# Kernel optimization log

Measured on AMD Instinct MI355X. Metric: run time of the kernel, lower is better.

The kernel has to match this reference:

```python
import jax, jax.numpy as jnp
import numpy as np

SEQ, BATCH, D_MODEL = 128, 64, 2048
D_STATE, D_CONV, CHUNK = 16, 4, 32
D_INNER = int(1.2 * D_MODEL)      # 2457
GROUPS = 7                        # largest g<=8 dividing 2457
DT_RANK = max(4, D_MODEL // 64)   # 32
WIN = 8
NEG = -1e30


def setup_inputs() -> dict:
    key = jax.random.key(0)
    ks = jax.random.split(key, 8)
    w = lambda k, shape, s: (jax.random.normal(k, shape) * s).astype(jnp.float32)
    return {
        "x": jax.random.normal(ks[0], (SEQ, BATCH, D_MODEL), dtype=jnp.float32),
        "W_in": w(ks[1], (D_INNER, D_MODEL), 0.02),
        "b_in": jnp.zeros((D_INNER,), jnp.float32),
        "W_gate": w(ks[2], (D_INNER, D_MODEL), 0.02),
        "b_gate": jnp.zeros((D_INNER,), jnp.float32),
        "W_conv": w(ks[3], (D_INNER, D_INNER // GROUPS, D_CONV), 0.05),
        "b_conv": jnp.zeros((D_INNER,), jnp.float32),
        "W_xproj": w(ks[4], (DT_RANK + D_STATE, D_INNER), 0.02),
        "b_xproj": jnp.zeros((DT_RANK + D_STATE,), jnp.float32),
        "W_dt": w(ks[5], (D_INNER, DT_RANK), 0.1),
        "Dparam": jnp.full((D_INNER,), 0.1, jnp.float32),
        "W_out": w(ks[6], (D_MODEL, D_INNER), 0.02),
        "b_out": jnp.zeros((D_MODEL,), jnp.float32),
        "ln_w": jnp.ones((D_MODEL,), jnp.float32),
        "ln_b": jnp.zeros((D_MODEL,), jnp.float32),
    }


def reference(x, W_in, b_in, W_gate, b_gate, W_conv, b_conv,
              W_xproj, b_xproj, W_dt, Dparam, W_out, b_out, ln_w, ln_b):
    def process_chunk(xc_in):                      # [L, B, d_model]
        L = xc_in.shape[0]
        xi = xc_in @ W_in.T + b_in                 # [L, B, d_inner]
        z = xc_in @ W_gate.T + b_gate              # gate
        # causal grouped conv1d: torch pads both sides by d_conv-1 then
        # truncates [:L]  ==  left-pad (d_conv-1), VALID conv
        c = jnp.transpose(xi, (1, 2, 0))           # [B, d_inner, L]
        c = jnp.pad(c, ((0, 0), (0, 0), (D_CONV - 1, 0)))
        c = jax.lax.conv_general_dilated(
            c, W_conv, window_strides=(1,), padding='VALID',
            dimension_numbers=('NCH', 'OIH', 'NCH'),
            feature_group_count=GROUPS) + b_conv[None, :, None]
        xc = jax.nn.silu(jnp.transpose(c, (2, 0, 1)))   # [L, B, d_inner]
        # dt_t = softplus(dt_proj(x_proj(x_t)[:dt_rank])) + 1e-4
        xp = xc @ W_xproj.T + b_xproj
        dt = jax.nn.softplus(xp[..., :DT_RANK] @ W_dt.T) + 1e-4  # [L,B,d_inner]
        xpad = jnp.pad(xc, ((WIN - 1, 0), (0, 0), (0, 0)))
        windows = jnp.stack([xpad[k:k + L] for k in range(WIN)], axis=1)
        t = jnp.arange(L)
        kk = jnp.arange(WIN)
        offset = jnp.maximum(0, WIN - 1 - t)       # shift so arange starts at 0
        ar = kk[None, :] - offset[:, None]
        valid = ar >= 0
        logits = dt[:, None] * ar[:, :, None, None].astype(dt.dtype)
        logits = jnp.where(valid[:, :, None, None], logits, NEG)
        wgt = jax.nn.softmax(logits, axis=1)       # softmax over window
        local = jnp.sum(wgt * windows, axis=1)     # [L, B, d_inner]
        return (local + Dparam * xc) * jax.nn.sigmoid(z)

    # chunks are processed independently (window + conv restart per chunk)
    xr = x.reshape(SEQ // CHUNK, CHUNK, BATCH, D_MODEL)
    ys = jax.vmap(process_chunk)(xr).reshape(SEQ, BATCH, D_INNER)
    compressed = ys[-WIN:].mean(axis=0)            # mean of last 8 steps
    out = compressed @ W_out.T + b_out             # [B, d_model]
    mu = out.mean(-1, keepdims=True)
    var = ((out - mu) ** 2).mean(-1, keepdims=True)
    return ((out - mu) / jnp.sqrt(var + 1e-5)) * ln_w + ln_b
```

## Files before the change

kernel.cpp:

```cpp
#include <hip/hip_runtime.h>
#include <math.h>
#include <stdint.h>

#define DMODEL 2048
#define DINNER 2457
#define NI     2464
#define GROUPS 7
#define GCH    351
#define GP     352
#define GNP    384
#define NROW_XI 1152
#define NROW_Z  512
#define NCAT   5120
#define GATE0  2560
#define OUT_SPLITS 16
#define CONV_PLANE (GROUPS * GNP * GP)

typedef __attribute__((ext_vector_type(8))) __bf16 bf16x8;
typedef __attribute__((ext_vector_type(4))) float f32x4;
typedef __attribute__((ext_vector_type(8))) unsigned short ushort8;

__device__ inline unsigned short f2bf(float f) {
    union { float f; unsigned int u; } v; v.f = f;
    unsigned int u = v.u;
    return (unsigned short)((u + 0x7FFFu + ((u >> 16) & 1u)) >> 16);
}

__device__ inline int lds_addr(int row, int slot) {
    return row * 32 + ((slot ^ ((row >> 1) & 3)) << 3);
}

__device__ __forceinline__ void gload16(const unsigned short* g, unsigned short* l) {
    __builtin_amdgcn_global_load_lds(
        (const __attribute__((address_space(1))) unsigned int*)g,
        (__attribute__((address_space(3))) unsigned int*)l, 16, 0, 0);
}

#define CAST_B0 1152
#define CAST_B1 6066
#define CAST_B2 9435
__global__ __launch_bounds__(256)
void cast_all(const float* __restrict__ x110,
              const float* __restrict__ Win, const float* __restrict__ Wg,
              const float* __restrict__ Wc,
              unsigned short* __restrict__ A_x,
              unsigned short* __restrict__ B_cat,
              unsigned short* __restrict__ B_cv)
{
    int bx = blockIdx.x;
    if (bx < CAST_B0) {
        size_t t = (size_t)bx * 256 + threadIdx.x;
        const float4* s = (const float4*)x110 + t * 2;
        float4 a = s[0], b = s[1];
        ushort8 o;
        o[0]=f2bf(a.x); o[1]=f2bf(a.y); o[2]=f2bf(a.z); o[3]=f2bf(a.w);
        o[4]=f2bf(b.x); o[5]=f2bf(b.y); o[6]=f2bf(b.z); o[7]=f2bf(b.w);
        *(ushort8*)(A_x + t * 8) = o;
    } else if (bx < CAST_B1) {
        int idx = bx - CAST_B0;
        int half = idx >= DINNER;
        int cb = half ? idx - DINNER : idx;
        const float* src = half ? Wg : Win;
        size_t t = (size_t)cb * 256 + threadIdx.x;
        size_t elem = t * 8;
        size_t doff = elem + (half ? (size_t)GATE0 * DMODEL : 0);
        const float4* s = (const float4*)(src + elem);
        float4 a = s[0], b = s[1];
        ushort8 o;
        o[0]=f2bf(a.x); o[1]=f2bf(a.y); o[2]=f2bf(a.z); o[3]=f2bf(a.w);
        o[4]=f2bf(b.x); o[5]=f2bf(b.y); o[6]=f2bf(b.z); o[7]=f2bf(b.w);
        *(ushort8*)(B_cat + doff) = o;
    } else {
        int t = (bx - CAST_B1) * 256 + threadIdx.x;
        if (t >= DINNER * GCH) return;
        int oc = t / GCH, i = t - oc * GCH;
        float4 w = *(const float4*)(Wc + (size_t)t * 4);
        int g = oc / GCH, ol = oc - g * GCH;
        size_t base = (size_t)(g * GNP + ol) * GP + i;
        B_cv[0 * (size_t)CONV_PLANE + base] = f2bf(w.x);
        B_cv[1 * (size_t)CONV_PLANE + base] = f2bf(w.y);
        B_cv[2 * (size_t)CONV_PLANE + base] = f2bf(w.z);
        B_cv[3 * (size_t)CONV_PLANE + base] = f2bf(w.w);
        if (i == GCH - 1) {
            B_cv[0 * (size_t)CONV_PLANE + base + 1] = 0;
            B_cv[1 * (size_t)CONV_PLANE + base + 1] = 0;
            B_cv[2 * (size_t)CONV_PLANE + base + 1] = 0;
            B_cv[3 * (size_t)CONV_PLANE + base + 1] = 0;
        }
    }
}

#define NKF 64
__global__ __launch_bounds__(256)
void gemm_mfma_fused(const unsigned short* __restrict__ A,
                     const unsigned short* __restrict__ B,
                     const float* __restrict__ b_in,
                     const float* __restrict__ b_gate,
                     unsigned short* __restrict__ xi,
                     float* __restrict__ zb)
{
    __shared__ unsigned short sm[5 * 256 * 32];
    const int tid = threadIdx.x;
    const int w = tid >> 6, l = tid & 63;
    const int l15 = l & 15, l4 = l >> 4;
    const int wm = w >> 1, wn = w & 1;

    const int orig = blockIdx.x;
    const int xcd = orig & 7, lo = orig >> 3;
    const int logical = (xcd < 4 ? xcd * 33 : 132 + (xcd - 4) * 32) + lo;
    int mt, nt, is_gate;
    if (logical < 180) { nt = logical / 9; mt = logical % 9; is_gate = 0; }
    else { int b2 = logical - 180; nt = 20 + b2 / 4; mt = 5 + b2 % 4; is_gate = 1; }
    const int m0 = mt * 128, n0 = nt * 128;

    const int lr = l >> 2, slot = l & 3;
    const int r0 = w * 16 + lr, r1 = r0 + 64;
    const int xo0 = (slot ^ ((r0 >> 1) & 3)) << 3;
    const int xo1 = (slot ^ ((r1 >> 1) & 3)) << 3;
    const unsigned short* gA0 = A + (size_t)(m0 + r0) * DMODEL + xo0;
    const unsigned short* gA1 = A + (size_t)(m0 + r1) * DMODEL + xo1;
    const unsigned short* gB0 = B + (size_t)(n0 + r0) * DMODEL + xo0;
    const unsigned short* gB1 = B + (size_t)(n0 + r1) * DMODEL + xo1;
    unsigned short* dA0 = sm + w * 512;
    unsigned short* dA1 = sm + (w + 4) * 512;
    unsigned short* dB0 = sm + 4096 + w * 512;
    unsigned short* dB1 = sm + 4096 + (w + 4) * 512;

#define STAGE_G(buf, ks) do { int _o = (ks) * 32, _b = (buf) * 8192; \
    gload16(gA0 + _o, dA0 + _b); gload16(gA1 + _o, dA1 + _b); \
    gload16(gB0 + _o, dB0 + _b); gload16(gB1 + _o, dB1 + _b); } while (0)

    f32x4 acc[4][4] = {};
    auto compute = [&](const unsigned short* base) {
        bf16x8 af[4], bfr[4];
#pragma unroll
        for (int f = 0; f < 4; ++f)
            af[f] = *(const bf16x8*)(base + lds_addr(wm * 64 + f * 16 + l15, l4));
#pragma unroll
        for (int j = 0; j < 4; ++j)
            bfr[j] = *(const bf16x8*)(base + 4096 + lds_addr(wn * 64 + j * 16 + l15, l4));
        __builtin_amdgcn_s_setprio(1);
#pragma unroll
        for (int i = 0; i < 4; ++i)
#pragma unroll
            for (int j = 0; j < 4; ++j)
                acc[i][j] = __builtin_amdgcn_mfma_f32_16x16x32_bf16(af[i], bfr[j], acc[i][j], 0, 0, 0);
        __builtin_amdgcn_s_setprio(0);
    };

    STAGE_G(0, 0); STAGE_G(1, 1); STAGE_G(2, 2); STAGE_G(3, 3);
    int rbuf = 0, sbuf = 4;
    for (int ks = 0; ks < NKF - 4; ++ks) {
        asm volatile("s_waitcnt vmcnt(12)" ::: "memory");
        __builtin_amdgcn_s_barrier();
        STAGE_G(sbuf, ks + 4);
        compute(sm + rbuf * 8192);
        rbuf = rbuf == 4 ? 0 : rbuf + 1;
        sbuf = sbuf == 4 ? 0 : sbuf + 1;
    }
    asm volatile("s_waitcnt vmcnt(12)" ::: "memory");
    __builtin_amdgcn_s_barrier();
    compute(sm + rbuf * 8192); rbuf = rbuf == 4 ? 0 : rbuf + 1;
    asm volatile("s_waitcnt vmcnt(8)" ::: "memory");
    __builtin_amdgcn_s_barrier();
    compute(sm + rbuf * 8192); rbuf = rbuf == 4 ? 0 : rbuf + 1;
    asm volatile("s_waitcnt vmcnt(4)" ::: "memory");
    __builtin_amdgcn_s_barrier();
    compute(sm + rbuf * 8192); rbuf = rbuf == 4 ? 0 : rbuf + 1;
    asm volatile("s_waitcnt vmcnt(0)" ::: "memory");
    __builtin_amdgcn_s_barrier();
    compute(sm + rbuf * 8192);
#undef STAGE_G

    if (!is_gate) {
#pragma unroll
        for (int j = 0; j < 4; ++j) {
            int colg = n0 + wn * 64 + j * 16 + l15;
            if (colg < DINNER) {
                int g = colg / GCH, ci = colg - g * GCH;
                float bias = b_in[colg];
                size_t dco = (size_t)(g * GP + ci);
#pragma unroll
                for (int i = 0; i < 4; ++i)
#pragma unroll
                    for (int r = 0; r < 4; ++r) {
                        int row = m0 + wm * 64 + i * 16 + l4 * 4 + r;
                        xi[(size_t)row * NI + dco] = f2bf(acc[i][j][r] + bias);
                        if (ci == GCH - 1) xi[(size_t)row * NI + dco + 1] = 0;
                    }
            }
        }
    } else {
#pragma unroll
        for (int j = 0; j < 4; ++j) {
            int ng = n0 + wn * 64 + j * 16 + l15 - GATE0;
            if (ng < DINNER) {
                float bias = b_gate[ng];
#pragma unroll
                for (int i = 0; i < 4; ++i)
#pragma unroll
                    for (int r = 0; r < 4; ++r) {
                        int row = m0 + wm * 64 + i * 16 + l4 * 4 + r;
                        zb[(size_t)(row - 640) * NI + ng] = acc[i][j][r] + bias;
                    }
            }
        }
    }
}

#define NKC 44
__global__ __launch_bounds__(256)
void conv_mfma(const unsigned short* __restrict__ xi,
               const unsigned short* __restrict__ Bc,
               const float* __restrict__ bc,
               float* __restrict__ xcb)
{
    __shared__ unsigned short sm[5 * 192 * 32];
    const int tid = threadIdx.x;
    const int w = tid >> 6, l = tid & 63;
    const int l15 = l & 15, l4 = l >> 4;
    const int wm = w >> 1, wn = w & 1;

    const int orig = blockIdx.x;
    const int xcd = orig & 7, lo = orig >> 3;
    const int logical = (xcd < 3 ? xcd * 40 : 120 + (xcd - 3) * 39) + lo;
    const int gn = logical / 15, mt = logical % 15;
    const int g = gn / 3, nt = gn % 3;
    const int m0 = mt * 64;
    const int n0l = nt * 128;

    const int lr = l >> 2, slot = l & 3;
    const int rA = w * 16 + lr;
    const int rB1 = rA + 64;
    const int xoA  = (slot ^ ((rA  >> 1) & 3)) << 3;
    const int xoB1 = (slot ^ ((rB1 >> 1) & 3)) << 3;
    const unsigned short* gAb = xi + (size_t)(m0 + rA) * NI + g * GP + xoA;
    const unsigned short* gB0 = Bc + (size_t)(g * GNP + n0l + rA) * GP + xoA;
    const unsigned short* gB1 = Bc + (size_t)(g * GNP + n0l + rB1) * GP + xoB1;
    unsigned short* dA  = sm + w * 512;
    unsigned short* dB0 = sm + 2048 + w * 512;
    unsigned short* dB1 = sm + 2048 + (w + 4) * 512;

#define STAGE_C(buf, ks) do { \
    int _tap = (ks) / 11, _kc = (ks) - _tap * 11, _b = (buf) * 6144; \
    size_t _ao = (size_t)(64 * _tap) * NI + _kc * 32; \
    size_t _bo = (size_t)_tap * CONV_PLANE + _kc * 32; \
    gload16(gAb + _ao, dA  + _b); \
    gload16(gB0 + _bo, dB0 + _b); \
    gload16(gB1 + _bo, dB1 + _b); } while (0)

    f32x4 acc[2][4] = {};
    auto compute = [&](const unsigned short* base) {
        bf16x8 af[2], bfr[4];
#pragma unroll
        for (int f = 0; f < 2; ++f)
            af[f] = *(const bf16x8*)(base + lds_addr(wm * 32 + f * 16 + l15, l4));
#pragma unroll
        for (int j = 0; j < 4; ++j)
            bfr[j] = *(const bf16x8*)(base + 2048 + lds_addr(wn * 64 + j * 16 + l15, l4));
        __builtin_amdgcn_s_setprio(1);
#pragma unroll
        for (int i = 0; i < 2; ++i)
#pragma unroll
            for (int j = 0; j < 4; ++j)
                acc[i][j] = __builtin_amdgcn_mfma_f32_16x16x32_bf16(af[i], bfr[j], acc[i][j], 0, 0, 0);
        __builtin_amdgcn_s_setprio(0);
    };

    STAGE_C(0, 0); STAGE_C(1, 1); STAGE_C(2, 2); STAGE_C(3, 3);
    int rbuf = 0, sbuf = 4;
    for (int ks = 0; ks < NKC - 4; ++ks) {
        asm volatile("s_waitcnt vmcnt(9)" ::: "memory");
        __builtin_amdgcn_s_barrier();
        STAGE_C(sbuf, ks + 4);
        compute(sm + rbuf * 6144);
        rbuf = rbuf == 4 ? 0 : rbuf + 1;
        sbuf = sbuf == 4 ? 0 : sbuf + 1;
    }
    asm volatile("s_waitcnt vmcnt(9)" ::: "memory");
    __builtin_amdgcn_s_barrier();
    compute(sm + rbuf * 6144); rbuf = rbuf == 4 ? 0 : rbuf + 1;
    asm volatile("s_waitcnt vmcnt(6)" ::: "memory");
    __builtin_amdgcn_s_barrier();
    compute(sm + rbuf * 6144); rbuf = rbuf == 4 ? 0 : rbuf + 1;
    asm volatile("s_waitcnt vmcnt(3)" ::: "memory");
    __builtin_amdgcn_s_barrier();
    compute(sm + rbuf * 6144); rbuf = rbuf == 4 ? 0 : rbuf + 1;
    asm volatile("s_waitcnt vmcnt(0)" ::: "memory");
    __builtin_amdgcn_s_barrier();
    compute(sm + rbuf * 6144);
#undef STAGE_C

#pragma unroll
    for (int j = 0; j < 4; ++j) {
        int ocl = n0l + wn * 64 + j * 16 + l15;
        if (ocl < GCH) {
            int ch = g * GCH + ocl;
            float bias = bc[ch];
#pragma unroll
            for (int i = 0; i < 2; ++i)
#pragma unroll
                for (int r = 0; r < 4; ++r) {
                    int row = m0 + wm * 32 + i * 16 + l4 * 4 + r;
                    float v = acc[i][j][r] + bias;
                    xcb[(size_t)row * NI + ch] = v / (1.f + expf(-v));
                }
        }
    }
}

__global__ __launch_bounds__(256)
void xp_kernel(const float* __restrict__ xc,
               const float* __restrict__ Wxp,
               const float* __restrict__ bxp,
               float* __restrict__ xp32)
{
    const int row = blockIdx.x;
    const float* a = xc + (size_t)(448 + row) * NI;
    float acc[32];
#pragma unroll
    for (int o = 0; o < 32; ++o) acc[o] = 0.f;
    for (int k = threadIdx.x; k < DINNER; k += 256) {
        float av = a[k];
#pragma unroll
        for (int o = 0; o < 32; ++o)
            acc[o] = fmaf(av, Wxp[(size_t)o * DINNER + k], acc[o]);
    }
#pragma unroll
    for (int o = 0; o < 32; ++o)
#pragma unroll
        for (int off = 32; off; off >>= 1)
            acc[o] += __shfl_down(acc[o], off);
    __shared__ float red[4][32];
    const int wid = threadIdx.x >> 6, lane = threadIdx.x & 63;
    if (lane == 0)
#pragma unroll
        for (int o = 0; o < 32; ++o) red[wid][o] = acc[o];
    __syncthreads();
    if (threadIdx.x < 32) {
        int o = threadIdx.x;
        xp32[row * 32 + o] = red[0][o] + red[1][o] + red[2][o] + red[3][o] + bxp[o];
    }
}

__global__ __launch_bounds__(256)
void fuse_kernel(const float* __restrict__ xc, const float* __restrict__ z,
                 const float* __restrict__ xp,
                 const float* __restrict__ Wdt,
                 const float* __restrict__ Dp,
                 float* __restrict__ comp)
{
    const int d = blockIdx.x * 256 + threadIdx.x;
    const int b = blockIdx.y;
    __shared__ float xps[8][32];
    {
        int s = threadIdx.x >> 5, o = threadIdx.x & 31;
        xps[s][o] = xp[((s * 64) + b) * 32 + o];
    }
    __syncthreads();
    if (d >= DINNER) return;
    float wd[32];
    {
        const float4* wp = (const float4*)(Wdt + (size_t)d * 32);
#pragma unroll
        for (int q = 0; q < 8; ++q) {
            float4 v = wp[q];
            wd[q * 4 + 0] = v.x; wd[q * 4 + 1] = v.y;
            wd[q * 4 + 2] = v.z; wd[q * 4 + 3] = v.w;
        }
    }
    float xcv[15];
#pragma unroll
    for (int tt = 0; tt < 15; ++tt) xcv[tt] = xc[(size_t)(tt * 64 + b) * NI + d];
    const float Dpd = Dp[d];
    float acc = 0.f;
#pragma unroll
    for (int s = 0; s < 8; ++s) {
        float sv = 0.f;
#pragma unroll
        for (int k = 0; k < 32; ++k) sv = fmaf(xps[s][k], wd[k], sv);
        float dval = fmaxf(sv, 0.f) + log1pf(expf(-fabsf(sv))) + 1e-4f;
        float zval = z[(size_t)(s * 64 + b) * NI + d];
        float e = expf(-dval);
        float w = 1.f, wsum = 0.f, lsum = 0.f;
#pragma unroll
        for (int k = 7; k >= 0; --k) {
            wsum += w;
            lsum = fmaf(w, xcv[s + k], lsum);
            w *= e;
        }
        float local = lsum / wsum;
        float ys = (local + Dpd * xcv[s + 7]) / (1.f + expf(-zval));
        acc += ys;
    }
    comp[(size_t)b * NI + d] = acc * 0.125f;
}

__global__ __launch_bounds__(256)
void gemm_nt_splitk(const float* __restrict__ A, int lda,
                    const float* __restrict__ B, int ldb,
                    float* __restrict__ Cp, int ldc,
                    int M, int N, int K, int kchunk)
{
    __shared__ float As[16][68];
    __shared__ float Bs[16][68];
    const int tid = threadIdx.x;
    const int tx = tid & 15, ty = tid >> 4;
    const int m0 = blockIdx.y * 64, n0 = blockIdx.x * 64;
    const int kbeg = blockIdx.z * kchunk;
    const int kend = min(K, kbeg + kchunk);
    float* C = Cp + (size_t)blockIdx.z * M * ldc;
    float acc[4][4] = {};
    for (int k0 = kbeg; k0 < kend; k0 += 16) {
#pragma unroll
        for (int u = 0; u < 4; ++u) {
            int idx = u * 256 + tid;
            int r = idx >> 4, kk = idx & 15;
            int gk = k0 + kk;
            float av = 0.f, bv = 0.f;
            if (gk < kend) {
                av = A[(size_t)(m0 + r) * lda + gk];
                int nn = n0 + r;
                bv = (nn < N) ? B[(size_t)nn * ldb + gk] : 0.f;
            }
            As[kk][r] = av;
            Bs[kk][r] = bv;
        }
        __syncthreads();
#pragma unroll
        for (int kk = 0; kk < 16; ++kk) {
            float4 a4 = *(const float4*)&As[kk][ty * 4];
            float4 b4 = *(const float4*)&Bs[kk][tx * 4];
            float a[4] = {a4.x, a4.y, a4.z, a4.w};
            float b[4] = {b4.x, b4.y, b4.z, b4.w};
#pragma unroll
            for (int i = 0; i < 4; ++i)
#pragma unroll
                for (int j = 0; j < 4; ++j)
                    acc[i][j] = fmaf(a[i], b[j], acc[i][j]);
        }
        __syncthreads();
    }
#pragma unroll
    for (int i = 0; i < 4; ++i) {
        int m = m0 + ty * 4 + i;
#pragma unroll
        for (int j = 0; j < 4; ++j) {
            int n = n0 + tx * 4 + j;
            if (n < N) C[(size_t)m * ldc + n] = acc[i][j];
        }
    }
}

__global__ __launch_bounds__(256)
void ln_kernel(const float* __restrict__ Cp,
               const float* __restrict__ b_out,
               const float* __restrict__ lw, const float* __restrict__ lb,
               float* __restrict__ out)
{
    const int b = blockIdx.x;
    const int tid = threadIdx.x;
    __shared__ float red[4];
    float v[8];
    float s = 0.f;
#pragma unroll
    for (int i = 0; i < 8; ++i) {
        int col = i * 256 + tid;
        float acc = b_out[col];
#pragma unroll
        for (int p = 0; p < OUT_SPLITS; ++p)
            acc += Cp[(size_t)p * 64 * 2048 + b * 2048 + col];
        v[i] = acc; s += acc;
    }
#pragma unroll
    for (int off = 32; off; off >>= 1) s += __shfl_down(s, off);
    if ((tid & 63) == 0) red[tid >> 6] = s;
    __syncthreads();
    float mu = (red[0] + red[1] + red[2] + red[3]) / 2048.f;
    float s2 = 0.f;
#pragma unroll
    for (int i = 0; i < 8; ++i) { float dd = v[i] - mu; s2 += dd * dd; }
#pragma unroll
    for (int off = 32; off; off >>= 1) s2 += __shfl_down(s2, off);
    __syncthreads();
    if ((tid & 63) == 0) red[tid >> 6] = s2;
    __syncthreads();
    float var = (red[0] + red[1] + red[2] + red[3]) / 2048.f;
    float inv = rsqrtf(var + 1e-5f);
#pragma unroll
    for (int i = 0; i < 8; ++i) {
        int dcol = i * 256 + tid;
        out[b * 2048 + dcol] = (v[i] - mu) * inv * lw[dcol] + lb[dcol];
    }
}

extern "C" void kernel_launch(void* const* d_in, const int* in_sizes, int n_in,
                              void* d_out, int out_size, void* d_ws, size_t ws_size,
                              hipStream_t stream)
{
    const float* x      = (const float*)d_in[0];
    const float* W_in   = (const float*)d_in[1];
    const float* b_in   = (const float*)d_in[2];
    const float* W_gate = (const float*)d_in[3];
    const float* b_gate = (const float*)d_in[4];
    const float* W_conv = (const float*)d_in[5];
    const float* b_conv = (const float*)d_in[6];
    const float* W_xp   = (const float*)d_in[7];
    const float* b_xp   = (const float*)d_in[8];
    const float* W_dt   = (const float*)d_in[9];
    const float* Dp     = (const float*)d_in[10];
    const float* W_out  = (const float*)d_in[11];
    const float* b_out  = (const float*)d_in[12];
    const float* ln_w   = (const float*)d_in[13];
    const float* ln_b   = (const float*)d_in[14];
    float* out = (float*)d_out;

    float* ws = (float*)d_ws;
    auto alloc = [&](size_t nf) { float* p = ws; ws += (nf + 255) & ~(size_t)255; return p; };
    unsigned short* A_x   = (unsigned short*)alloc((size_t)NROW_XI * DMODEL / 2);
    unsigned short* B_cat = (unsigned short*)alloc((size_t)NCAT * DMODEL / 2);
    unsigned short* B_cv  = (unsigned short*)alloc((size_t)4 * CONV_PLANE / 2);
    unsigned short* xi_bf = (unsigned short*)alloc((size_t)NROW_XI * NI / 2);
    float* zb   = alloc((size_t)NROW_Z * NI);
    float* xp32 = alloc((size_t)512 * 32);
    float* comp = alloc((size_t)64 * NI);
    float* xcb     = (float*)B_cat;
    float* outpart = (float*)B_cat + (size_t)960 * NI;

    cast_all<<<CAST_B2, 256, 0, stream>>>(x + (size_t)(110 * 64) * DMODEL,
                                          W_in, W_gate, W_conv, A_x, B_cat, B_cv);
    gemm_mfma_fused<<<260, 256, 0, stream>>>(A_x, B_cat, b_in, b_gate, xi_bf, zb);
    conv_mfma<<<315, 256, 0, stream>>>(xi_bf, B_cv, b_conv, xcb);
    xp_kernel<<<512, 256, 0, stream>>>(xcb, W_xp, b_xp, xp32);
    {
        dim3 grid((DINNER + 255) / 256, 64);
        fuse_kernel<<<grid, 256, 0, stream>>>(xcb, zb, xp32, W_dt, Dp, comp);
    }
    {
        const int kchunk = (DINNER + OUT_SPLITS - 1) / OUT_SPLITS;
        dim3 grid(DMODEL / 64, 1, OUT_SPLITS);
        gemm_nt_splitk<<<grid, 256, 0, stream>>>(comp, NI, W_out, DINNER,
                                                 outpart, DMODEL, 64, DMODEL, DINNER, kchunk);
    }
    ln_kernel<<<64, 256, 0, stream>>>(outpart, b_out, ln_w, ln_b, out);
}
```

Baseline: 126.8 us.

## Merge tail kernels pairwise using software grid barriers

The xp projection and the fuse stage become one kernel, and the split-K output GEMM and LayerNorm become another. Inside each kernel the two stages are separated by an atomic-counter grid barrier, and the counters are zeroed by a memset before the launches. This removes two kernel launches and their gaps. It relies on all 512 blocks being co-resident; if they are not, the barrier deadlocks, and the spin-wait adds its own latency.

```diff
diff --git a/kernel.cpp b/kernel.cpp
--- a/kernel.cpp
+++ b/kernel.cpp
@@ -34,6 +34,17 @@
     __builtin_amdgcn_global_load_lds(
         (const __attribute__((address_space(1))) unsigned int*)g,
         (__attribute__((address_space(3))) unsigned int*)l, 16, 0, 0);
+}
+
+__device__ __forceinline__ void grid_barrier(unsigned* cnt, unsigned nb) {
+    __syncthreads();
+    if (threadIdx.x == 0) {
+        __threadfence();
+        atomicAdd(cnt, 1u);
+        while (atomicAdd(cnt, 0u) < nb) __builtin_amdgcn_s_sleep(8);
+        __threadfence();
+    }
+    __syncthreads();
 }
 
 #define CAST_B0 1152
@@ -310,156 +321,155 @@
 }
 
 __global__ __launch_bounds__(256)
-void xp_kernel(const float* __restrict__ xc,
-               const float* __restrict__ Wxp,
-               const float* __restrict__ bxp,
-               float* __restrict__ xp32)
+void xp_fuse(const float* __restrict__ xc,
+             const float* __restrict__ Wxp,
+             const float* __restrict__ bxp,
+             const float* __restrict__ z,
+             const float* __restrict__ Wdt,
+             const float* __restrict__ Dp,
+             float* __restrict__ xp32,
+             float* __restrict__ comp,
+             unsigned* __restrict__ barcnt)
 {
-    const int row = blockIdx.x;
-    const float* a = xc + (size_t)(448 + row) * NI;
-    float acc[32];
-#pragma unroll
-    for (int o = 0; o < 32; ++o) acc[o] = 0.f;
-    for (int k = threadIdx.x; k < DINNER; k += 256) {
-        float av = a[k];
+    {
+        const int row = blockIdx.x;
+        const float* a = xc + (size_t)(448 + row) * NI;
+        float acc[32];
+#pragma unroll
+        for (int o = 0; o < 32; ++o) acc[o] = 0.f;
+        for (int k = threadIdx.x; k < DINNER; k += 256) {
+            float av = a[k];
+#pragma unroll
+            for (int o = 0; o < 32; ++o)
+                acc[o] = fmaf(av, Wxp[(size_t)o * DINNER + k], acc[o]);
+        }
 #pragma unroll
         for (int o = 0; o < 32; ++o)
-            acc[o] = fmaf(av, Wxp[(size_t)o * DINNER + k], acc[o]);
-    }
-#pragma unroll
-    for (int o = 0; o < 32; ++o)
-#pragma unroll
-        for (int off = 32; off; off >>= 1)
-            acc[o] += __shfl_down(acc[o], off);
-    __shared__ float red[4][32];
-    const int wid = threadIdx.x >> 6, lane = threadIdx.x & 63;
-    if (lane == 0)
-#pragma unroll
-        for (int o = 0; o < 32; ++o) red[wid][o] = acc[o];
-    __syncthreads();
-    if (threadIdx.x < 32) {
-        int o = threadIdx.x;
-        xp32[row * 32 + o] = red[0][o] + red[1][o] + red[2][o] + red[3][o] + bxp[o];
+#pragma unroll
+            for (int off = 32; off; off >>= 1)
+                acc[o] += __shfl_down(acc[o], off);
+        __shared__ float red[4][32];
+        const int wid = threadIdx.x >> 6, lane = threadIdx.x & 63;
+        if (lane == 0)
+#pragma unroll
+            for (int o = 0; o < 32; ++o) red[wid][o] = acc[o];
+        __syncthreads();
+        if (threadIdx.x < 32) {
+            int o = threadIdx.x;
+            xp32[row * 32 + o] = red[0][o] + red[1][o] + red[2][o] + red[3][o] + bxp[o];
+        }
+    }
+    grid_barrier(barcnt, 512);
+    __shared__ float xps[8][32];
+    for (int lb = blockIdx.x; lb < 640; lb += 512) {
+        const int dx = lb % 10, b = lb / 10;
+        __syncthreads();
+        {
+            int s = threadIdx.x >> 5, o = threadIdx.x & 31;
+            xps[s][o] = xp32[((s * 64) + b) * 32 + o];
+        }
+        __syncthreads();
+        const int d = dx * 256 + threadIdx.x;
+        if (d >= DINNER) continue;
+        float wd[32];
+        {
+            const float4* wp = (const float4*)(Wdt + (size_t)d * 32);
+#pragma unroll
+            for (int q = 0; q < 8; ++q) {
+                float4 v = wp[q];
+                wd[q * 4 + 0] = v.x; wd[q * 4 + 1] = v.y;
+                wd[q * 4 + 2] = v.z; wd[q * 4 + 3] = v.w;
+            }
+        }
+        float xcv[15];
+#pragma unroll
+        for (int tt = 0; tt < 15; ++tt) xcv[tt] = xc[(size_t)(tt * 64 + b) * NI + d];
+        const float Dpd = Dp[d];
+        float acc = 0.f;
+#pragma unroll
+        for (int s = 0; s < 8; ++s) {
+            float sv = 0.f;
+#pragma unroll
+            for (int k = 0; k < 32; ++k) sv = fmaf(xps[s][k], wd[k], sv);
+            float dval = fmaxf(sv, 0.f) + log1pf(expf(-fabsf(sv))) + 1e-4f;
+            float zval = z[(size_t)(s * 64 + b) * NI + d];
+            float e = expf(-dval);
+            float w = 1.f, wsum = 0.f, lsum = 0.f;
+#pragma unroll
+            for (int k = 7; k >= 0; --k) {
+                wsum += w;
+                lsum = fmaf(w, xcv[s + k], lsum);
+                w *= e;
+            }
+            float local = lsum / wsum;
+            float ys = (local + Dpd * xcv[s + 7]) / (1.f + expf(-zval));
+            acc += ys;
+        }
+        comp[(size_t)b * NI + d] = acc * 0.125f;
     }
 }
 
 __global__ __launch_bounds__(256)
-void fuse_kernel(const float* __restrict__ xc, const float* __restrict__ z,
-                 const float* __restrict__ xp,
-                 const float* __restrict__ Wdt,
-                 const float* __restrict__ Dp,
-                 float* __restrict__ comp)
-{
-    const int d = blockIdx.x * 256 + threadIdx.x;
-    const int b = blockIdx.y;
-    __shared__ float xps[8][32];
-    {
-        int s = threadIdx.x >> 5, o = threadIdx.x & 31;
-        xps[s][o] = xp[((s * 64) + b) * 32 + o];
-    }
-    __syncthreads();
-    if (d >= DINNER) return;
-    float wd[32];
-    {
-        const float4* wp = (const float4*)(Wdt + (size_t)d * 32);
-#pragma unroll
-        for (int q = 0; q < 8; ++q) {
-            float4 v = wp[q];
-            wd[q * 4 + 0] = v.x; wd[q * 4 + 1] = v.y;
-            wd[q * 4 + 2] = v.z; wd[q * 4 + 3] = v.w;
-        }
-    }
-    float xcv[15];
-#pragma unroll
-    for (int tt = 0; tt < 15; ++tt) xcv[tt] = xc[(size_t)(tt * 64 + b) * NI + d];
-    const float Dpd = Dp[d];
-    float acc = 0.f;
-#pragma unroll
-    for (int s = 0; s < 8; ++s) {
-        float sv = 0.f;
-#pragma unroll
-        for (int k = 0; k < 32; ++k) sv = fmaf(xps[s][k], wd[k], sv);
-        float dval = fmaxf(sv, 0.f) + log1pf(expf(-fabsf(sv))) + 1e-4f;
-        float zval = z[(size_t)(s * 64 + b) * NI + d];
-        float e = expf(-dval);
-        float w = 1.f, wsum = 0.f, lsum = 0.f;
-#pragma unroll
-        for (int k = 7; k >= 0; --k) {
-            wsum += w;
-            lsum = fmaf(w, xcv[s + k], lsum);
-            w *= e;
-        }
-        float local = lsum / wsum;
-        float ys = (local + Dpd * xcv[s + 7]) / (1.f + expf(-zval));
-        acc += ys;
-    }
-    comp[(size_t)b * NI + d] = acc * 0.125f;
-}
-
-__global__ __launch_bounds__(256)
-void gemm_nt_splitk(const float* __restrict__ A, int lda,
-                    const float* __restrict__ B, int ldb,
-                    float* __restrict__ Cp, int ldc,
-                    int M, int N, int K, int kchunk)
+void splitk_ln(const float* __restrict__ A,
+               const float* __restrict__ B,
+               float* __restrict__ Cp,
+               const float* __restrict__ b_out,
+               const float* __restrict__ lw, const float* __restrict__ lb,
+               float* __restrict__ out,
+               unsigned* __restrict__ barcnt)
 {
     __shared__ float As[16][68];
     __shared__ float Bs[16][68];
     const int tid = threadIdx.x;
-    const int tx = tid & 15, ty = tid >> 4;
-    const int m0 = blockIdx.y * 64, n0 = blockIdx.x * 64;
-    const int kbeg = blockIdx.z * kchunk;
-    const int kend = min(K, kbeg + kchunk);
-    float* C = Cp + (size_t)blockIdx.z * M * ldc;
-    float acc[4][4] = {};
-    for (int k0 = kbeg; k0 < kend; k0 += 16) {
-#pragma unroll
-        for (int u = 0; u < 4; ++u) {
-            int idx = u * 256 + tid;
-            int r = idx >> 4, kk = idx & 15;
-            int gk = k0 + kk;
-            float av = 0.f, bv = 0.f;
-            if (gk < kend) {
-                av = A[(size_t)(m0 + r) * lda + gk];
-                int nn = n0 + r;
-                bv = (nn < N) ? B[(size_t)nn * ldb + gk] : 0.f;
+    {
+        const int tx = tid & 15, ty = tid >> 4;
+        const int nt = blockIdx.x & 31, sp = blockIdx.x >> 5;
+        const int n0 = nt * 64;
+        const int kchunk = (DINNER + OUT_SPLITS - 1) / OUT_SPLITS;
+        const int kbeg = sp * kchunk;
+        const int kend = min(DINNER, kbeg + kchunk);
+        float* C = Cp + (size_t)sp * 64 * 2048;
+        float acc[4][4] = {};
+        for (int k0 = kbeg; k0 < kend; k0 += 16) {
+#pragma unroll
+            for (int u = 0; u < 4; ++u) {
+                int idx = u * 256 + tid;
+                int r = idx >> 4, kk = idx & 15;
+                int gk = k0 + kk;
+                float av = 0.f, bv = 0.f;
+                if (gk < kend) {
+                    av = A[(size_t)r * NI + gk];
+                    bv = B[(size_t)(n0 + r) * DINNER + gk];
+                }
+                As[kk][r] = av;
+                Bs[kk][r] = bv;
             }
-            As[kk][r] = av;
-            Bs[kk][r] = bv;
-        }
-        __syncthreads();
-#pragma unroll
-        for (int kk = 0; kk < 16; ++kk) {
-            float4 a4 = *(const float4*)&As[kk][ty * 4];
-            float4 b4 = *(const float4*)&Bs[kk][tx * 4];
-            float a[4] = {a4.x, a4.y, a4.z, a4.w};
-            float b[4] = {b4.x, b4.y, b4.z, b4.w};
-#pragma unroll
-            for (int i = 0; i < 4; ++i)
-#pragma unroll
-                for (int j = 0; j < 4; ++j)
-                    acc[i][j] = fmaf(a[i], b[j], acc[i][j]);
-        }
-        __syncthreads();
-    }
-#pragma unroll
-    for (int i = 0; i < 4; ++i) {
-        int m = m0 + ty * 4 + i;
-#pragma unroll
-        for (int j = 0; j < 4; ++j) {
-            int n = n0 + tx * 4 + j;
-            if (n < N) C[(size_t)m * ldc + n] = acc[i][j];
-        }
-    }
-}
-
-__global__ __launch_bounds__(256)
-void ln_kernel(const float* __restrict__ Cp,
-               const float* __restrict__ b_out,
-               const float* __restrict__ lw, const float* __restrict__ lb,
-               float* __restrict__ out)
-{
+            __syncthreads();
+#pragma unroll
+            for (int kk = 0; kk < 16; ++kk) {
+                float4 a4 = *(const float4*)&As[kk][ty * 4];
+                float4 b4 = *(const float4*)&Bs[kk][tx * 4];
+                float a[4] = {a4.x, a4.y, a4.z, a4.w};
+                float b[4] = {b4.x, b4.y, b4.z, b4.w};
+#pragma unroll
+                for (int i = 0; i < 4; ++i)
+#pragma unroll
+                    for (int j = 0; j < 4; ++j)
+                        acc[i][j] = fmaf(a[i], b[j], acc[i][j]);
+            }
+            __syncthreads();
+        }
+#pragma unroll
+        for (int i = 0; i < 4; ++i) {
+            int m = ty * 4 + i;
+#pragma unroll
+            for (int j = 0; j < 4; ++j)
+                C[(size_t)m * 2048 + n0 + tx * 4 + j] = acc[i][j];
+        }
+    }
+    grid_barrier(barcnt, 512);
+    if (blockIdx.x >= 64) return;
     const int b = blockIdx.x;
-    const int tid = threadIdx.x;
     __shared__ float red[4];
     float v[8];
     float s = 0.f;
@@ -524,23 +534,17 @@
     float* zb   = alloc((size_t)NROW_Z * NI);
     float* xp32 = alloc((size_t)512 * 32);
     float* comp = alloc((size_t)64 * NI);
+    unsigned* barcnt = (unsigned*)alloc(256);
     float* xcb     = (float*)B_cat;
     float* outpart = (float*)B_cat + (size_t)960 * NI;
 
+    hipMemsetAsync(barcnt, 0, 1024, stream);
     cast_all<<<CAST_B2, 256, 0, stream>>>(x + (size_t)(110 * 64) * DMODEL,
                                           W_in, W_gate, W_conv, A_x, B_cat, B_cv);
     gemm_mfma_fused<<<260, 256, 0, stream>>>(A_x, B_cat, b_in, b_gate, xi_bf, zb);
     conv_mfma<<<315, 256, 0, stream>>>(xi_bf, B_cv, b_conv, xcb);
-    xp_kernel<<<512, 256, 0, stream>>>(xcb, W_xp, b_xp, xp32);
-    {
-        dim3 grid((DINNER + 255) / 256, 64);
-        fuse_kernel<<<grid, 256, 0, stream>>>(xcb, zb, xp32, W_dt, Dp, comp);
-    }
-    {
-        const int kchunk = (DINNER + OUT_SPLITS - 1) / OUT_SPLITS;
-        dim3 grid(DMODEL / 64, 1, OUT_SPLITS);
-        gemm_nt_splitk<<<grid, 256, 0, stream>>>(comp, NI, W_out, DINNER,
-                                                 outpart, DMODEL, 64, DMODEL, DINNER, kchunk);
-    }
-    ln_kernel<<<64, 256, 0, stream>>>(outpart, b_out, ln_w, ln_b, out);
-}
+    xp_fuse<<<512, 256, 0, stream>>>(xcb, W_xp, b_xp, zb, W_dt, Dp, xp32, comp,
+                                     barcnt);
+    splitk_ln<<<512, 256, 0, stream>>>(comp, W_out, outpart, b_out, ln_w, ln_b,
+                                       out, barcnt + 64);
+}
```

Result: slower. 205.8 us (+62.3%).

## Overlap conv-weight cast with GEMM and fuse x_proj into conv epilogue

Applied to the files above, without the earlier changes.

Moves the grouped-conv weight bf16 cast out of the cast kernel into extra blocks of the fused GEMM launch, so it can run on CUs left idle by the 260 GEMM tiles. Removes the separate xp_kernel: conv blocks covering the final rows compute partial x_proj dot products over their channel slice and write 21 partials, which fuse_kernel sums along with the bias. This drops one launch and a full re-read of xc rows, but adds a serial scalar dot-product loop to the conv tail and extra partial-sum traffic.

```diff
diff --git a/kernel.cpp b/kernel.cpp
--- a/kernel.cpp
+++ b/kernel.cpp
@@ -38,14 +38,11 @@
 
 #define CAST_B0 1152
 #define CAST_B1 6066
-#define CAST_B2 9435
 __global__ __launch_bounds__(256)
 void cast_all(const float* __restrict__ x110,
               const float* __restrict__ Win, const float* __restrict__ Wg,
-              const float* __restrict__ Wc,
               unsigned short* __restrict__ A_x,
-              unsigned short* __restrict__ B_cat,
-              unsigned short* __restrict__ B_cv)
+              unsigned short* __restrict__ B_cat)
 {
     int bx = blockIdx.x;
     if (bx < CAST_B0) {
@@ -56,7 +53,7 @@
         o[0]=f2bf(a.x); o[1]=f2bf(a.y); o[2]=f2bf(a.z); o[3]=f2bf(a.w);
         o[4]=f2bf(b.x); o[5]=f2bf(b.y); o[6]=f2bf(b.z); o[7]=f2bf(b.w);
         *(ushort8*)(A_x + t * 8) = o;
-    } else if (bx < CAST_B1) {
+    } else {
         int idx = bx - CAST_B0;
         int half = idx >= DINNER;
         int cb = half ? idx - DINNER : idx;
@@ -70,42 +67,51 @@
         o[0]=f2bf(a.x); o[1]=f2bf(a.y); o[2]=f2bf(a.z); o[3]=f2bf(a.w);
         o[4]=f2bf(b.x); o[5]=f2bf(b.y); o[6]=f2bf(b.z); o[7]=f2bf(b.w);
         *(ushort8*)(B_cat + doff) = o;
-    } else {
-        int t = (bx - CAST_B1) * 256 + threadIdx.x;
-        if (t >= DINNER * GCH) return;
-        int oc = t / GCH, i = t - oc * GCH;
-        float4 w = *(const float4*)(Wc + (size_t)t * 4);
-        int g = oc / GCH, ol = oc - g * GCH;
-        size_t base = (size_t)(g * GNP + ol) * GP + i;
-        B_cv[0 * (size_t)CONV_PLANE + base] = f2bf(w.x);
-        B_cv[1 * (size_t)CONV_PLANE + base] = f2bf(w.y);
-        B_cv[2 * (size_t)CONV_PLANE + base] = f2bf(w.z);
-        B_cv[3 * (size_t)CONV_PLANE + base] = f2bf(w.w);
-        if (i == GCH - 1) {
-            B_cv[0 * (size_t)CONV_PLANE + base + 1] = 0;
-            B_cv[1 * (size_t)CONV_PLANE + base + 1] = 0;
-            B_cv[2 * (size_t)CONV_PLANE + base + 1] = 0;
-            B_cv[3 * (size_t)CONV_PLANE + base + 1] = 0;
-        }
     }
 }
 
 #define NKF 64
+#define GEMM_BLKS 260
+#define CAST_BLKS 224
 __global__ __launch_bounds__(256)
 void gemm_mfma_fused(const unsigned short* __restrict__ A,
                      const unsigned short* __restrict__ B,
+                     const float* __restrict__ Wc,
                      const float* __restrict__ b_in,
                      const float* __restrict__ b_gate,
                      unsigned short* __restrict__ xi,
-                     float* __restrict__ zb)
+                     float* __restrict__ zb,
+                     unsigned short* __restrict__ B_cv)
 {
     __shared__ unsigned short sm[5 * 256 * 32];
     const int tid = threadIdx.x;
+    const int orig = blockIdx.x;
+
+    if (orig >= GEMM_BLKS) {
+        for (int t = (orig - GEMM_BLKS) * 256 + tid; t < DINNER * GCH;
+             t += CAST_BLKS * 256) {
+            int oc = t / GCH, i = t - oc * GCH;
+            float4 w4 = *(const float4*)(Wc + (size_t)t * 4);
+            int g = oc / GCH, ol = oc - g * GCH;
+            size_t base = (size_t)(g * GNP + ol) * GP + i;
+            B_cv[0 * (size_t)CONV_PLANE + base] = f2bf(w4.x);
+            B_cv[1 * (size_t)CONV_PLANE + base] = f2bf(w4.y);
+            B_cv[2 * (size_t)CONV_PLANE + base] = f2bf(w4.z);
+            B_cv[3 * (size_t)CONV_PLANE + base] = f2bf(w4.w);
+            if (i == GCH - 1) {
+                B_cv[0 * (size_t)CONV_PLANE + base + 1] = 0;
+                B_cv[1 * (size_t)CONV_PLANE + base + 1] = 0;
+                B_cv[2 * (size_t)CONV_PLANE + base + 1] = 0;
+                B_cv[3 * (size_t)CONV_PLANE + base + 1] = 0;
+            }
+        }
+        return;
+    }
+
     const int w = tid >> 6, l = tid & 63;
     const int l15 = l & 15, l4 = l >> 4;
     const int wm = w >> 1, wn = w & 1;
 
-    const int orig = blockIdx.x;
     const int xcd = orig & 7, lo = orig >> 3;
     const int logical = (xcd < 4 ? xcd * 33 : 132 + (xcd - 4) * 32) + lo;
     int mt, nt, is_gate;
@@ -213,7 +219,9 @@
 void conv_mfma(const unsigned short* __restrict__ xi,
                const unsigned short* __restrict__ Bc,
                const float* __restrict__ bc,
-               float* __restrict__ xcb)
+               const float* __restrict__ Wxp,
+               float* __restrict__ xcb,
+               float* __restrict__ xp_part)
 {
     __shared__ unsigned short sm[5 * 192 * 32];
     const int tid = threadIdx.x;
@@ -307,45 +315,30 @@
                 }
         }
     }
-}
-
-__global__ __launch_bounds__(256)
-void xp_kernel(const float* __restrict__ xc,
-               const float* __restrict__ Wxp,
-               const float* __restrict__ bxp,
-               float* __restrict__ xp32)
-{
-    const int row = blockIdx.x;
-    const float* a = xc + (size_t)(448 + row) * NI;
-    float acc[32];
-#pragma unroll
-    for (int o = 0; o < 32; ++o) acc[o] = 0.f;
-    for (int k = threadIdx.x; k < DINNER; k += 256) {
-        float av = a[k];
-#pragma unroll
-        for (int o = 0; o < 32; ++o)
-            acc[o] = fmaf(av, Wxp[(size_t)o * DINNER + k], acc[o]);
-    }
-#pragma unroll
-    for (int o = 0; o < 32; ++o)
-#pragma unroll
-        for (int off = 32; off; off >>= 1)
-            acc[o] += __shfl_down(acc[o], off);
-    __shared__ float red[4][32];
-    const int wid = threadIdx.x >> 6, lane = threadIdx.x & 63;
-    if (lane == 0)
-#pragma unroll
-        for (int o = 0; o < 32; ++o) red[wid][o] = acc[o];
-    __syncthreads();
-    if (threadIdx.x < 32) {
-        int o = threadIdx.x;
-        xp32[row * 32 + o] = red[0][o] + red[1][o] + red[2][o] + red[3][o] + bxp[o];
+
+    if (m0 >= 448) {
+        __syncthreads();
+        const int o  = tid & 31;
+        const int rg = tid >> 5;
+        const int cmax = (GCH - n0l) < 128 ? (GCH - n0l) : 128;
+        const float* wrow = Wxp + (size_t)o * DINNER + g * GCH + n0l;
+        float* dst = xp_part + ((size_t)(g * 3 + nt) * 512 + (m0 - 448)) * 32;
+#pragma unroll
+        for (int q = 0; q < 8; ++q) {
+            int rl = rg * 8 + q;
+            const float* xrow = xcb + (size_t)(m0 + rl) * NI + g * GCH + n0l;
+            float s = 0.f;
+            for (int c = 0; c < cmax; ++c)
+                s = fmaf(xrow[c], wrow[c], s);
+            dst[(size_t)rl * 32 + o] = s;
+        }
     }
 }
 
 __global__ __launch_bounds__(256)
 void fuse_kernel(const float* __restrict__ xc, const float* __restrict__ z,
-                 const float* __restrict__ xp,
+                 const float* __restrict__ xp_part,
+                 const float* __restrict__ bxp,
                  const float* __restrict__ Wdt,
                  const float* __restrict__ Dp,
                  float* __restrict__ comp)
@@ -355,7 +348,12 @@
     __shared__ float xps[8][32];
     {
         int s = threadIdx.x >> 5, o = threadIdx.x & 31;
-        xps[s][o] = xp[((s * 64) + b) * 32 + o];
+        int row = s * 64 + b;
+        float v = bxp[o];
+#pragma unroll
+        for (int p = 0; p < 21; ++p)
+            v += xp_part[((size_t)p * 512 + row) * 32 + o];
+        xps[s][o] = v;
     }
     __syncthreads();
     if (d >= DINNER) return;
@@ -521,20 +519,20 @@
     unsigned short* B_cat = (unsigned short*)alloc((size_t)NCAT * DMODEL / 2);
     unsigned short* B_cv  = (unsigned short*)alloc((size_t)4 * CONV_PLANE / 2);
     unsigned short* xi_bf = (unsigned short*)alloc((size_t)NROW_XI * NI / 2);
-    float* zb   = alloc((size_t)NROW_Z * NI);
-    float* xp32 = alloc((size_t)512 * 32);
-    float* comp = alloc((size_t)64 * NI);
+    float* zb      = alloc((size_t)NROW_Z * NI);
+    float* xp_part = alloc((size_t)21 * 512 * 32);
+    float* comp    = alloc((size_t)64 * NI);
     float* xcb     = (float*)B_cat;
     float* outpart = (float*)B_cat + (size_t)960 * NI;
 
-    cast_all<<<CAST_B2, 256, 0, stream>>>(x + (size_t)(110 * 64) * DMODEL,
-                                          W_in, W_gate, W_conv, A_x, B_cat, B_cv);
-    gemm_mfma_fused<<<260, 256, 0, stream>>>(A_x, B_cat, b_in, b_gate, xi_bf, zb);
-    conv_mfma<<<315, 256, 0, stream>>>(xi_bf, B_cv, b_conv, xcb);
-    xp_kernel<<<512, 256, 0, stream>>>(xcb, W_xp, b_xp, xp32);
+    cast_all<<<CAST_B1, 256, 0, stream>>>(x + (size_t)(110 * 64) * DMODEL,
+                                          W_in, W_gate, A_x, B_cat);
+    gemm_mfma_fused<<<GEMM_BLKS + CAST_BLKS, 256, 0, stream>>>(
+        A_x, B_cat, W_conv, b_in, b_gate, xi_bf, zb, B_cv);
+    conv_mfma<<<315, 256, 0, stream>>>(xi_bf, B_cv, b_conv, W_xp, xcb, xp_part);
     {
         dim3 grid((DINNER + 255) / 256, 64);
-        fuse_kernel<<<grid, 256, 0, stream>>>(xcb, zb, xp32, W_dt, Dp, comp);
+        fuse_kernel<<<grid, 256, 0, stream>>>(xcb, zb, xp_part, b_xp, W_dt, Dp, comp);
     }
     {
         const int kchunk = (DINNER + OUT_SPLITS - 1) / OUT_SPLITS;
```

Measured after the change: 290.2 us. 2.29x slower.

## Move conv weight cast into GEMM launch as extra blocks to overlap

Applied to the files above, without the earlier changes.

The conv-weight bf16 cast moves out of the front-loaded cast kernel and runs as 224 extra grid-stride blocks appended to the fused input/gate GEMM launch. The GEMM uses only 260 blocks on a 256-CU device, so the extra blocks can fill idle CUs while the GEMM runs, which shortens the critical path of the cast kernel. The risk is that the cast blocks compete with the GEMM for memory bandwidth and CU slots, and the GEMM kernel now carries extra arguments and a branch.

```diff
diff --git a/kernel.cpp b/kernel.cpp
--- a/kernel.cpp
+++ b/kernel.cpp
@@ -38,14 +38,11 @@
 
 #define CAST_B0 1152
 #define CAST_B1 6066
-#define CAST_B2 9435
 __global__ __launch_bounds__(256)
 void cast_all(const float* __restrict__ x110,
               const float* __restrict__ Win, const float* __restrict__ Wg,
-              const float* __restrict__ Wc,
               unsigned short* __restrict__ A_x,
-              unsigned short* __restrict__ B_cat,
-              unsigned short* __restrict__ B_cv)
+              unsigned short* __restrict__ B_cat)
 {
     int bx = blockIdx.x;
     if (bx < CAST_B0) {
@@ -56,7 +53,7 @@
         o[0]=f2bf(a.x); o[1]=f2bf(a.y); o[2]=f2bf(a.z); o[3]=f2bf(a.w);
         o[4]=f2bf(b.x); o[5]=f2bf(b.y); o[6]=f2bf(b.z); o[7]=f2bf(b.w);
         *(ushort8*)(A_x + t * 8) = o;
-    } else if (bx < CAST_B1) {
+    } else {
         int idx = bx - CAST_B0;
         int half = idx >= DINNER;
         int cb = half ? idx - DINNER : idx;
@@ -70,42 +67,51 @@
         o[0]=f2bf(a.x); o[1]=f2bf(a.y); o[2]=f2bf(a.z); o[3]=f2bf(a.w);
         o[4]=f2bf(b.x); o[5]=f2bf(b.y); o[6]=f2bf(b.z); o[7]=f2bf(b.w);
         *(ushort8*)(B_cat + doff) = o;
-    } else {
-        int t = (bx - CAST_B1) * 256 + threadIdx.x;
-        if (t >= DINNER * GCH) return;
-        int oc = t / GCH, i = t - oc * GCH;
-        float4 w = *(const float4*)(Wc + (size_t)t * 4);
-        int g = oc / GCH, ol = oc - g * GCH;
-        size_t base = (size_t)(g * GNP + ol) * GP + i;
-        B_cv[0 * (size_t)CONV_PLANE + base] = f2bf(w.x);
-        B_cv[1 * (size_t)CONV_PLANE + base] = f2bf(w.y);
-        B_cv[2 * (size_t)CONV_PLANE + base] = f2bf(w.z);
-        B_cv[3 * (size_t)CONV_PLANE + base] = f2bf(w.w);
-        if (i == GCH - 1) {
-            B_cv[0 * (size_t)CONV_PLANE + base + 1] = 0;
-            B_cv[1 * (size_t)CONV_PLANE + base + 1] = 0;
-            B_cv[2 * (size_t)CONV_PLANE + base + 1] = 0;
-            B_cv[3 * (size_t)CONV_PLANE + base + 1] = 0;
-        }
     }
 }
 
 #define NKF 64
+#define GEMM_BLKS 260
+#define CAST_BLKS 224
 __global__ __launch_bounds__(256)
 void gemm_mfma_fused(const unsigned short* __restrict__ A,
                      const unsigned short* __restrict__ B,
+                     const float* __restrict__ Wc,
                      const float* __restrict__ b_in,
                      const float* __restrict__ b_gate,
                      unsigned short* __restrict__ xi,
-                     float* __restrict__ zb)
+                     float* __restrict__ zb,
+                     unsigned short* __restrict__ B_cv)
 {
     __shared__ unsigned short sm[5 * 256 * 32];
     const int tid = threadIdx.x;
+    const int orig = blockIdx.x;
+
+    if (orig >= GEMM_BLKS) {
+        for (int t = (orig - GEMM_BLKS) * 256 + tid; t < DINNER * GCH;
+             t += CAST_BLKS * 256) {
+            int oc = t / GCH, i = t - oc * GCH;
+            float4 w4 = *(const float4*)(Wc + (size_t)t * 4);
+            int g = oc / GCH, ol = oc - g * GCH;
+            size_t base = (size_t)(g * GNP + ol) * GP + i;
+            B_cv[0 * (size_t)CONV_PLANE + base] = f2bf(w4.x);
+            B_cv[1 * (size_t)CONV_PLANE + base] = f2bf(w4.y);
+            B_cv[2 * (size_t)CONV_PLANE + base] = f2bf(w4.z);
+            B_cv[3 * (size_t)CONV_PLANE + base] = f2bf(w4.w);
+            if (i == GCH - 1) {
+                B_cv[0 * (size_t)CONV_PLANE + base + 1] = 0;
+                B_cv[1 * (size_t)CONV_PLANE + base + 1] = 0;
+                B_cv[2 * (size_t)CONV_PLANE + base + 1] = 0;
+                B_cv[3 * (size_t)CONV_PLANE + base + 1] = 0;
+            }
+        }
+        return;
+    }
+
     const int w = tid >> 6, l = tid & 63;
     const int l15 = l & 15, l4 = l >> 4;
     const int wm = w >> 1, wn = w & 1;
 
-    const int orig = blockIdx.x;
     const int xcd = orig & 7, lo = orig >> 3;
     const int logical = (xcd < 4 ? xcd * 33 : 132 + (xcd - 4) * 32) + lo;
     int mt, nt, is_gate;
@@ -527,9 +533,10 @@
     float* xcb     = (float*)B_cat;
     float* outpart = (float*)B_cat + (size_t)960 * NI;
 
-    cast_all<<<CAST_B2, 256, 0, stream>>>(x + (size_t)(110 * 64) * DMODEL,
-                                          W_in, W_gate, W_conv, A_x, B_cat, B_cv);
-    gemm_mfma_fused<<<260, 256, 0, stream>>>(A_x, B_cat, b_in, b_gate, xi_bf, zb);
+    cast_all<<<CAST_B1, 256, 0, stream>>>(x + (size_t)(110 * 64) * DMODEL,
+                                          W_in, W_gate, A_x, B_cat);
+    gemm_mfma_fused<<<GEMM_BLKS + CAST_BLKS, 256, 0, stream>>>(
+        A_x, B_cat, W_conv, b_in, b_gate, xi_bf, zb, B_cv);
     conv_mfma<<<315, 256, 0, stream>>>(xi_bf, B_cv, b_conv, xcb);
     xp_kernel<<<512, 256, 0, stream>>>(xcb, W_xp, b_xp, xp32);
     {
```

New measurement: 124.1 us. 1.02x faster.
